# Kernel optimization log

Hardware: AMD Instinct MI355X
Metric: run time of the kernel (lower is better)

Reference implementation:

```python
import jax, jax.numpy as jnp
import numpy as np
from jax import lax

B, L, R = 128, 256, 36
D_TXT, D_IMG, D_SOC = 768, 2048, 10
EPS = 0.05 ** 2        # geomloss blur=0.05, p=2 -> epsilon = blur^p
N_ITERS = 20           # fixed log-domain Sinkhorn iterations
GAMMA = 0.01


def _pcost(x, y):
    # x: [B,n,d], y: [B,m,d] -> C_ij = ||x_i - y_j||^2 / 2 (geomloss p=2 cost)
    xx = jnp.sum(x * x, -1)[:, :, None]
    yy = jnp.sum(y * y, -1)[:, None, :]
    xy = jnp.einsum('bnd,bmd->bnm', x, y)
    return 0.5 * (xx + yy - 2.0 * xy)


def _sinkhorn_cost(C, loga, logb, eps, n_iters):
    # Log-domain Sinkhorn; masked points carry loga/logb = -inf (zero weight).
    f = jnp.zeros(loga.shape, C.dtype)
    g = jnp.zeros(logb.shape, C.dtype)

    def body(fg, _):
        f, g = fg
        g = -eps * jax.nn.logsumexp(loga[:, :, None] + (f[:, :, None] - C) / eps, axis=1)
        f = -eps * jax.nn.logsumexp(logb[:, None, :] + (g[:, None, :] - C) / eps, axis=2)
        return (f, g), None

    (f, g), _ = lax.scan(body, (f, g), None, length=n_iters)
    a = jnp.exp(loga)  # exp(-inf) = 0 for masked entries
    b = jnp.exp(logb)
    return jnp.sum(a * f, -1) + jnp.sum(b * g, -1)  # <a,f> + <b,g>


def _forward(txt_global, txt_region, img_global, img_region, social, attn_mask,
             W_stat, b_stat, W_gt, b_gt, W_gi, b_gi, W_rt, b_rt, W_ri, b_ri,
             W_m1, b_m1, W_m2, b_m2):
    relu = jax.nn.relu
    soc = relu(social @ W_stat + b_stat)                            # [B,100]
    tg = relu(jnp.concatenate([txt_global, soc], axis=1) @ W_gt + b_gt)  # [B,200]
    ig = relu(img_global @ W_gi + b_gi)                              # [B,200]
    h = relu((tg + ig) @ W_m1 + b_m1)
    mix_pred = h @ W_m2 + b_m2                                       # [B,2]

    tr = relu(txt_region @ W_rt + b_rt)                              # [B,L,50]
    ir = relu(img_region @ W_ri + b_ri)                              # [B,R,50]

    Bn, _, _ = tr.shape
    Rn = ir.shape[1]
    mask = attn_mask > 0
    n_words = jnp.sum(attn_mask, axis=-1).astype(tr.dtype)          # [B]
    loga = jnp.where(mask, -jnp.log(n_words)[:, None], -jnp.inf)    # uniform over valid tokens
    logb = jnp.full((Bn, Rn), -jnp.log(float(Rn)), tr.dtype)        # uniform over regions

    # Debiased Sinkhorn divergence (geomloss SamplesLoss default debias=True):
    Sxy = _sinkhorn_cost(_pcost(tr, ir), loga, logb, EPS, N_ITERS)
    Sxx = _sinkhorn_cost(_pcost(tr, tr), loga, loga, EPS, N_ITERS)
    Syy = _sinkhorn_cost(_pcost(ir, ir), logb, logb, EPS, N_ITERS)
    w_dis = Sxy - 0.5 * (Sxx + Syy)                                  # [B]

    w_pred = jnp.stack([1.0 - GAMMA * w_dis, GAMMA * w_dis], axis=1)  # [B,2]
    logit = jax.nn.softmax(jnp.maximum(mix_pred, w_pred), axis=1)
    return logit


def setup_inputs() -> dict:
    key = jax.random.key(0)
    ks = jax.random.split(key, 24)
    init = lambda k, s: (jax.random.normal(k, s) * 0.02).astype(jnp.float32)
    lengths = jax.random.randint(ks[0], (B,), 16, L + 1)             # ragged lengths
    attn_mask = (jnp.arange(L)[None, :] < lengths[:, None]).astype(jnp.int32)
    return {
        'txt_global': jax.random.normal(ks[1], (B, D_TXT), jnp.float32),
        'txt_region': jax.random.normal(ks[2], (B, L, D_TXT), jnp.float32),
        'img_global': jax.random.normal(ks[3], (B, D_IMG), jnp.float32),
        'img_region': jax.random.normal(ks[4], (B, R, D_IMG), jnp.float32),
        'social': jax.random.normal(ks[5], (B, D_SOC), jnp.float32),
        'attn_mask': attn_mask,
        'W_stat': init(ks[6], (D_SOC, 100)), 'b_stat': jnp.zeros((100,), jnp.float32),
        'W_gt': init(ks[7], (868, 200)), 'b_gt': jnp.zeros((200,), jnp.float32),
        'W_gi': init(ks[8], (D_IMG, 200)), 'b_gi': jnp.zeros((200,), jnp.float32),
        'W_rt': init(ks[9], (D_TXT, 50)), 'b_rt': jnp.zeros((50,), jnp.float32),
        'W_ri': init(ks[10], (D_IMG, 50)), 'b_ri': jnp.zeros((50,), jnp.float32),
        'W_m1': init(ks[11], (200, 100)), 'b_m1': jnp.zeros((100,), jnp.float32),
        'W_m2': init(ks[12], (100, 2)), 'b_m2': jnp.zeros((2,), jnp.float32),
    }


def reference(txt_global, txt_region, img_global, img_region, social, attn_mask,
              W_stat, b_stat, W_gt, b_gt, W_gi, b_gi, W_rt, b_rt, W_ri, b_ri,
              W_m1, b_m1, W_m2, b_m2):
    return _forward(txt_global, txt_region, img_global, img_region, social, attn_mask,
                    W_stat, b_stat, W_gt, b_gt, W_gi, b_gi, W_rt, b_rt, W_ri, b_ri,
                    W_m1, b_m1, W_m2, b_m2)
```

## Files before the change

### kernel.cpp

```cpp
#include <hip/hip_runtime.h>

typedef float  f32x4 __attribute__((ext_vector_type(4)));
typedef short  s16x8 __attribute__((ext_vector_type(8)));

#define EPS_LN2      0.0017328679513998632f
#define INV_EPS_LN2  577.0780163555852f
#define LOG2_36      5.169925001442312f

__device__ __forceinline__ short f2bf(float x) {
  unsigned int u; __builtin_memcpy(&u, &x, 4);
  u = (u + 0x7FFFu + ((u >> 16) & 1u)) >> 16;
  return (short)u;
}

#define GLOAD16(g, l) __builtin_amdgcn_global_load_lds( \
    (const __attribute__((address_space(1))) void*)(g), \
    (__attribute__((address_space(3))) void*)(l), 16, 0, 0)

__global__ __launch_bounds__(256) void k_prep(
    const float* __restrict__ W_rt, const float* __restrict__ W_ri,
    short* __restrict__ frt, short* __restrict__ fri,
    const float* __restrict__ txt, const float* __restrict__ img,
    const float* __restrict__ social,
    const float* __restrict__ W_stat, const float* __restrict__ b_stat,
    const float* __restrict__ W_gt, const float* __restrict__ W_gi,
    float* __restrict__ pre) {
  __shared__ float sA[32][128];
  int bid = blockIdx.x;
  if (bid < 88) {
    int slot = bid * 256 + threadIdx.x;
    const float* W; short* dst; int f;
    if (slot < 6144) { W = W_rt; dst = frt; f = slot; }
    else             { W = W_ri; dst = fri; f = slot - 6144; }
    int k32 = f >> 8, rem = f & 255, ct = rem >> 6, l = rem & 63;
    int col = ct * 16 + (l & 15);
    int k0  = k32 * 32 + (l >> 4) * 8;
    s16x8 p;
#pragma unroll
    for (int c = 0; c < 8; ++c) {
      float v = (col < 50) ? W[(k0 + c) * 50 + col] : 0.f;
      p[c] = f2bf(v);
    }
    *(s16x8*)(dst + (long)f * 8) = p;
    return;
  }
  int gb = bid - 88;
  int job = gb >> 4, rb = (gb >> 2) & 3, cb = gb & 3;
  int t = threadIdx.x, r0 = rb * 32;
  const float* W; int k0, klen;
  if (job < 6)       { k0 = job * 128;       klen = 128; W = W_gt; }
  else if (job == 6) { k0 = 0;               klen = 100; W = W_gt + 768 * 200; }
  else               { k0 = (job - 7) * 128; klen = 128; W = W_gi; }
  if (job == 6) {
    for (int idx = t; idx < 4096; idx += 256) {
      int r = idx >> 7, k = idx & 127;
      float v = 0.f;
      if (k < 100) {
        v = b_stat[k];
#pragma unroll
        for (int u = 0; u < 10; ++u) v += social[(r0 + r) * 10 + u] * W_stat[u * 100 + k];
        v = fmaxf(v, 0.f);
      }
      sA[r][k] = v;
    }
  } else {
    const float* A = (job < 6) ? txt : img;
    int K_A = (job < 6) ? 768 : 2048;
    for (int idx = t; idx < 4096; idx += 256) {
      int r = idx >> 7, k = idx & 127;
      sA[r][k] = A[(r0 + r) * K_A + k0 + k];
    }
  }
  __syncthreads();
  int c = cb * 64 + (t & 63), rg = t >> 6;
  if (c < 200) {
    float acc[8];
#pragma unroll
    for (int i = 0; i < 8; ++i) acc[i] = 0.f;
    for (int k4 = 0; k4 < klen; k4 += 4) {
      float w0 = W[(k0 + k4    ) * 200 + c];
      float w1 = W[(k0 + k4 + 1) * 200 + c];
      float w2 = W[(k0 + k4 + 2) * 200 + c];
      float w3 = W[(k0 + k4 + 3) * 200 + c];
#pragma unroll
      for (int i = 0; i < 8; ++i) {
        f32x4 a = *(const f32x4*)&sA[rg * 8 + i][k4];
        acc[i] += a[0]*w0 + a[1]*w1 + a[2]*w2 + a[3]*w3;
      }
    }
    float* dst = pre + (long)job * 25600;
#pragma unroll
    for (int i = 0; i < 8; ++i)
      dst[(r0 + rg * 8 + i) * 200 + c] = acc[i];
  }
}

template<int K32>
__device__ __forceinline__ void proj_body(const float* __restrict__ A,
                                          const short* __restrict__ Bf,
                                          const float* __restrict__ bias,
                                          float* __restrict__ out, int bid,
                                          char* smem) {
  char* abuf = smem;
  char* bbuf = smem + 16384;
  int wave = threadIdx.x >> 6, lane = threadIdx.x & 63;
  int rl = lane & 15, q = lane >> 4;
  int row0 = bid * 64;
  const int K = K32 * 32;
  const float* arow = A + (long)(row0 + wave * 16 + rl) * K + q * 8;
  const short* brow = Bf + wave * 512 + lane * 8;

#define PROJ_STAGE(KK, PH) { \
    const float* asrc = arow + (KK) * 32; \
    char* ad = abuf + (PH) * 8192 + wave * 2048; \
    GLOAD16(asrc,     ad); \
    GLOAD16(asrc + 4, ad + 1024); \
    GLOAD16(brow + (long)(KK) * 2048, bbuf + (PH) * 4096 + wave * 1024); \
  }

  f32x4 acc[4];
#pragma unroll
  for (int ct = 0; ct < 4; ++ct) acc[ct] = (f32x4){0.f, 0.f, 0.f, 0.f};

  PROJ_STAGE(0, 0);
  __syncthreads();

  for (int k = 0; k < K32; ++k) {
    if (k + 1 < K32) PROJ_STAGE(k + 1, (k + 1) & 1);
    const char* ab = abuf + (k & 1) * 8192 + wave * 2048 + lane * 16;
    const char* bb = bbuf + (k & 1) * 4096 + lane * 16;
    f32x4 a0 = *(const f32x4*)(ab);
    f32x4 a1 = *(const f32x4*)(ab + 1024);
    s16x8 af;
    af[0]=f2bf(a0[0]); af[1]=f2bf(a0[1]); af[2]=f2bf(a0[2]); af[3]=f2bf(a0[3]);
    af[4]=f2bf(a1[0]); af[5]=f2bf(a1[1]); af[6]=f2bf(a1[2]); af[7]=f2bf(a1[3]);
#pragma unroll
    for (int ct = 0; ct < 4; ++ct) {
      s16x8 bfr = *(const s16x8*)(bb + ct * 1024);
      acc[ct] = __builtin_amdgcn_mfma_f32_16x16x32_bf16(af, bfr, acc[ct], 0, 0, 0);
    }
    __syncthreads();
  }
#undef PROJ_STAGE

#pragma unroll
  for (int ct = 0; ct < 4; ++ct) {
    int col = ct * 16 + rl;
    float bv = (col < 50) ? bias[col] : 0.f;
#pragma unroll
    for (int r = 0; r < 4; ++r) {
      int grow = row0 + wave * 16 + q * 4 + r;
      float v = fmaxf(acc[ct][r] + bv, 0.f);
      out[(long)grow * 64 + col] = (col < 50) ? v : 0.f;
    }
  }
}

__device__ __forceinline__ void mix_body(
    int r, const float* __restrict__ pre,
    const float* __restrict__ b_gt, const float* __restrict__ b_gi,
    const float* __restrict__ W_m1, const float* __restrict__ b_m1,
    const float* __restrict__ W_m2, const float* __restrict__ b_m2,
    float* __restrict__ mix, float* smem) {
  float* sm = smem;
  float* sh = smem + 200;
  int t = threadIdx.x;
  if (t < 200) {
    float s1 = b_gt[t], s2 = b_gi[t];
#pragma unroll
    for (int j = 0; j < 7; ++j)  s1 += pre[(long)j * 25600 + r * 200 + t];
#pragma unroll
    for (int j = 7; j < 23; ++j) s2 += pre[(long)j * 25600 + r * 200 + t];
    sm[t] = fmaxf(s1, 0.f) + fmaxf(s2, 0.f);
  }
  __syncthreads();
  if (t < 100) {
    float a = b_m1[t];
#pragma unroll 4
    for (int k = 0; k < 200; ++k) a += sm[k] * W_m1[k * 100 + t];
    sh[t] = fmaxf(a, 0.f);
  }
  __syncthreads();
  if (t < 2) {
    float a = b_m2[t];
    for (int k = 0; k < 100; ++k) a += sh[k] * W_m2[k * 2 + t];
    mix[r * 2 + t] = a;
  }
}

__global__ __launch_bounds__(256)
void k_pm(
    const float* __restrict__ txt_region, const short* __restrict__ frt,
    const float* __restrict__ b_rt, float* __restrict__ tr,
    const float* __restrict__ img_region, const short* __restrict__ fri,
    const float* __restrict__ b_ri, float* __restrict__ ir,
    const float* __restrict__ pre,
    const float* __restrict__ b_gt, const float* __restrict__ b_gi,
    const float* __restrict__ W_m1, const float* __restrict__ b_m1,
    const float* __restrict__ W_m2, const float* __restrict__ b_m2,
    float* __restrict__ mix) {
  __shared__ __align__(16) char smem[24576];
  int bid = blockIdx.x;
  if (bid < 72)       proj_body<64>(img_region, fri, b_ri, ir, bid, smem);
  else if (bid < 584) proj_body<24>(txt_region, frt, b_rt, tr, bid - 72, smem);
  else                mix_body(bid - 584, pre, b_gt, b_gi, W_m1, b_m1, W_m2, b_m2, mix, (float*)smem);
}

#define SK_SMEM 50736

__global__ __launch_bounds__(1024)
__attribute__((amdgpu_waves_per_eu(4, 4)))
void k_sink(
    const float* __restrict__ tr, const float* __restrict__ ir,
    const int* __restrict__ amask, float* __restrict__ Cxx,
    float* __restrict__ Sxy, float* __restrict__ Sxx, float* __restrict__ Syy) {
  __shared__ __align__(16) char smem[SK_SMEM];
  int role = blockIdx.x >> 7;
  int b    = blockIdx.x & 127;
  int tid  = threadIdx.x;

  if (role == 0) {
    short* Xf    = (short*)smem;
    float* norms = (float*)(smem + 32768);
    float* sA    = (float*)(smem + 33792);
    float* sF    = (float*)(smem + 34816);
    float* sG    = (float*)(smem + 35840);
    float* sPm   = (float*)(smem + 36864);
    int*   nsh   = (int*)  (smem + 40960);
    if (tid < 64) {
      int c = 0;
      for (int i = tid; i < 256; i += 64) c += amask[b * 256 + i];
#pragma unroll
      for (int o = 1; o < 64; o <<= 1) c += __shfl_xor(c, o);
      if (tid == 0) *nsh = c;
    }
    const float* Xg = tr + (long)b * 256 * 64;
    for (int slot = tid; slot < 2048; slot += 1024) {
      int t = slot >> 7, k32 = (slot >> 6) & 1, l = slot & 63;
      int row = t * 16 + (l & 15), k0 = k32 * 32 + (l >> 4) * 8;
      const float* src = Xg + row * 64 + k0;
      f32x4 a0 = *(const f32x4*)src, a1 = *(const f32x4*)(src + 4);
      s16x8 p;
      p[0]=f2bf(a0[0]); p[1]=f2bf(a0[1]); p[2]=f2bf(a0[2]); p[3]=f2bf(a0[3]);
      p[4]=f2bf(a1[0]); p[5]=f2bf(a1[1]); p[6]=f2bf(a1[2]); p[7]=f2bf(a1[3]);
      *(s16x8*)(Xf + slot * 8) = p;
    }
    __syncthreads();
    int n = *nsh;
    int wv = tid >> 6, lane = tid & 63, q = lane >> 4;
    f32x4 acc[16];
#pragma unroll
    for (int ct = 0; ct < 16; ++ct) acc[ct] = (f32x4){0.f, 0.f, 0.f, 0.f};
    s16x8 afr0 = *(const s16x8*)(Xf + ((wv * 2 + 0) * 64 + lane) * 8);
    s16x8 afr1 = *(const s16x8*)(Xf + ((wv * 2 + 1) * 64 + lane) * 8);
#pragma unroll
    for (int ct = 0; ct < 16; ++ct) {
      s16x8 b0 = *(const s16x8*)(Xf + ((ct * 2 + 0) * 64 + lane) * 8);
      s16x8 b1 = *(const s16x8*)(Xf + ((ct * 2 + 1) * 64 + lane) * 8);
      acc[ct] = __builtin_amdgcn_mfma_f32_16x16x32_bf16(afr0, b0, acc[ct], 0, 0, 0);
      acc[ct] = __builtin_amdgcn_mfma_f32_16x16x32_bf16(afr1, b1, acc[ct], 0, 0, 0);
    }
#pragma unroll
    for (int r = 0; r < 4; ++r) {
      int m_ = q * 4 + r;
      if ((lane & 15) == m_) norms[wv * 16 + m_] = acc[wv][r];
    }
    __syncthreads();
    float* Cwb = Cxx + (long)b * 65536;
    if (wv * 16 < n) {
#pragma unroll
      for (int ct = 0; ct < 16; ++ct) {
        int gj = ct * 16 + (lane & 15);
        float nj = norms[gj];
#pragma unroll
        for (int r = 0; r < 4; ++r) {
          int gi = wv * 16 + q * 4 + r;
          Cwb[gi * 256 + gj] = (acc[ct][r] - 0.5f * (norms[gi] + nj)) * INV_EPS_LN2;
        }
      }
    }
    __syncthreads();
    int kk = tid >> 8, j = tid & 255, i0 = kk * 64;
    int iend = n - i0; if (iend > 64) iend = 64;
    f32x4 c0, c1, c2, c3, c4, c5, c6, c7, c8, c9, ca, cb, cc, cd, ce, cf;
    if (i0 < n) {
      const float* cp = Cwb + (long)i0 * 256 + j;
#define XXLD(CV, T0) \
      CV[0] = cp[(T0+0)*256]; CV[1] = cp[(T0+1)*256]; \
      CV[2] = cp[(T0+2)*256]; CV[3] = cp[(T0+3)*256];
      XXLD(c0, 0)  XXLD(c1, 4)  XXLD(c2, 8)  XXLD(c3, 12)
      XXLD(c4, 16) XXLD(c5, 20) XXLD(c6, 24) XXLD(c7, 28)
      XXLD(c8, 32) XXLD(c9, 36) XXLD(ca, 40) XXLD(cb, 44)
      XXLD(cc, 48) XXLD(cd, 52) XXLD(ce, 56) XXLD(cf, 60)
#undef XXLD
      asm volatile("" : "+v"(c0), "+v"(c1), "+v"(c2), "+v"(c3),
                        "+v"(c4), "+v"(c5), "+v"(c6), "+v"(c7),
                        "+v"(c8), "+v"(c9), "+v"(ca), "+v"(cb),
                        "+v"(cc), "+v"(cd), "+v"(ce), "+v"(cf));
    }
    float log2n = log2f((float)n);
    if (tid < 256) { sF[tid] = 0.f; sA[tid] = (tid < n) ? -log2n : -1e30f; }
    __syncthreads();
    const float* ap2 = sA + i0;
#define XXG(CA, CB, CC, CD, OFF) { \
      f32x4 A0 = *(const f32x4*)(ap2 + OFF); \
      f32x4 A1 = *(const f32x4*)(ap2 + OFF + 4); \
      f32x4 A2 = *(const f32x4*)(ap2 + OFF + 8); \
      f32x4 A3 = *(const f32x4*)(ap2 + OFF + 12); \
      float x0 = A0[0]+CA[0], x1 = A0[1]+CA[1], x2 = A0[2]+CA[2], x3 = A0[3]+CA[3]; \
      float x4 = A1[0]+CB[0], x5 = A1[1]+CB[1], x6 = A1[2]+CB[2], x7 = A1[3]+CB[3]; \
      float x8 = A2[0]+CC[0], x9 = A2[1]+CC[1], xa = A2[2]+CC[2], xb = A2[3]+CC[3]; \
      float xc = A3[0]+CD[0], xd = A3[1]+CD[1], xe = A3[2]+CD[2], xf = A3[3]+CD[3]; \
      float y0 = fmaxf(fmaxf(x0, x1), x2); \
      float y1 = fmaxf(fmaxf(x3, x4), x5); \
      float y2 = fmaxf(fmaxf(x6, x7), x8); \
      float y3 = fmaxf(fmaxf(x9, xa), xb); \
      float y4 = fmaxf(fmaxf(xc, xd), xe); \
      m = fmaxf(m, fmaxf(fmaxf(fmaxf(y0, y1), fmaxf(y2, y3)), fmaxf(y4, xf))); }
    for (int h = 0; h < 40; ++h) {
      float m = -1e30f;
      if (i0 < n && j < n) {
        XXG(c0, c1, c2, c3, 0)
        if (iend > 16) { XXG(c4, c5, c6, c7, 16) }
        if (iend > 32) { XXG(c8, c9, ca, cb, 32) }
        if (iend > 48) { XXG(cc, cd, ce, cf, 48) }
      }
      sPm[kk * 256 + j] = m;
      __syncthreads();
      if (tid < 256) {
        float m4 = fmaxf(fmaxf(sPm[tid], sPm[256 + tid]),
                         fmaxf(sPm[512 + tid], sPm[768 + tid]));
        if (tid < n) {
          ((h & 1) ? sF : sG)[tid] = -EPS_LN2 * m4;
          sA[tid] = -log2n - m4;
        }
      }
      __syncthreads();
    }
#undef XXG
    if (tid < 64) {
      float a = 0.f;
      for (int i = tid; i < n; i += 64) a += sF[i] + sG[i];
#pragma unroll
      for (int o = 1; o < 64; o <<= 1) a += __shfl_xor(a, o);
      if (tid == 0) Sxx[b] = a / n;
    }
  } else if (role == 1) {
    float* Ys  = (float*)smem;
    float* Cs  = (float*)(smem + 9216);
    float* nx  = (float*)(smem + 47104);
    float* ny  = (float*)(smem + 48128);
    float* sA  = (float*)(smem + 48288);
    float* sB  = (float*)(smem + 49376);
    float* sF  = (float*)(smem + 49536);
    float* sG  = (float*)(smem + 50560);
    int*   nsh = (int*)  (smem + 50720);
    if (tid < 64) {
      int c = 0;
      for (int i = tid; i < 256; i += 64) c += amask[b * 256 + i];
#pragma unroll
      for (int o = 1; o < 64; o <<= 1) c += __shfl_xor(c, o);
      if (tid == 0) *nsh = c;
    }
    const float* Xg = tr + (long)b * 256 * 64;
    const float* Yg = ir + (long)b * 36 * 64;
    for (int idx = tid; idx < 576; idx += 1024) {
      int row = idx >> 4, q4 = idx & 15;
      *(f32x4*)(Ys + row * 64 + q4 * 4) = *(const f32x4*)(Yg + row * 64 + q4 * 4);
    }
    __syncthreads();
    int n = *nsh;
    if (tid < 256) {
      float a = 0.f;
#pragma unroll
      for (int q4 = 0; q4 < 13; ++q4) {
        f32x4 v = *(const f32x4*)(Xg + tid * 64 + q4 * 4);
        a += v[0]*v[0] + v[1]*v[1] + v[2]*v[2] + v[3]*v[3];
      }
      nx[tid] = a;
    } else if (tid < 292) {
      int jj = tid - 256; float a = 0.f;
#pragma unroll
      for (int q4 = 0; q4 < 13; ++q4) {
        f32x4 v = *(const f32x4*)(Ys + jj * 64 + q4 * 4);
        a += v[0]*v[0] + v[1]*v[1] + v[2]*v[2] + v[3]*v[3];
      }
      ny[jj] = a;
    }
    __syncthreads();
    if (tid < 1008) {
      int ii = tid / 36, jj = tid - ii * 36;
      f32x4 yr[13];
#pragma unroll
      for (int q4 = 0; q4 < 13; ++q4) yr[q4] = *(const f32x4*)(Ys + jj * 64 + q4 * 4);
      float nyj = ny[jj];
      for (int i = ii; i < 256; i += 28) {
        float d = 0.f;
#pragma unroll
        for (int q4 = 0; q4 < 13; ++q4) {
          f32x4 xv = *(const f32x4*)(Xg + i * 64 + q4 * 4);
          d += xv[0]*yr[q4][0] + xv[1]*yr[q4][1] + xv[2]*yr[q4][2] + xv[3]*yr[q4][3];
        }
        Cs[i * 37 + jj] = (d - 0.5f * (nx[i] + nyj)) * INV_EPS_LN2;
      }
    }
    __syncthreads();
    int jg = tid >> 4, kg = tid & 15;
    float Cg[16];
    if (jg < 36) {
#pragma unroll
      for (int t = 0; t < 16; ++t) Cg[t] = Cs[(kg * 16 + t) * 37 + jg];
    }
    int fi = tid >> 2, kf = tid & 3;
    float Cf[9];
#pragma unroll
    for (int t = 0; t < 9; ++t) {
      int jj2 = kf * 9 + t;
      Cf[t] = (jj2 < 36) ? Cs[fi * 37 + jj2] : 0.f;
    }
    float log2n = log2f((float)n);
    if (tid < 256) { sF[tid] = 0.f; sA[tid + (tid >> 4)] = -log2n; }
    __syncthreads();
    const float* agp = sA + kg * 17;
    int gend = n - kg * 16; if (gend > 16) gend = 16;
    for (int it = 0; it < 20; ++it) {
      float gm = -1e30f;
      if (jg < 36) {
#pragma unroll
        for (int t = 0; t < 16; ++t)
          if (t < gend) gm = fmaxf(gm, agp[t] + Cg[t]);
        gm = fmaxf(gm, __shfl_xor(gm, 1)); gm = fmaxf(gm, __shfl_xor(gm, 2));
        gm = fmaxf(gm, __shfl_xor(gm, 4)); gm = fmaxf(gm, __shfl_xor(gm, 8));
      }
      __syncthreads();
      if (jg < 36 && kg == 0) {
        sG[jg] = -EPS_LN2 * gm;
        sB[jg] = -LOG2_36 - gm;
      }
      __syncthreads();
      float fm = -1e30f;
#pragma unroll
      for (int t = 0; t < 9; ++t) {
        int jj2 = kf * 9 + t;
        if (jj2 < 36) fm = fmaxf(fm, sB[jj2] + Cf[t]);
      }
      fm = fmaxf(fm, __shfl_xor(fm, 1)); fm = fmaxf(fm, __shfl_xor(fm, 2));
      __syncthreads();
      if (kf == 0 && fi < n) {
        sF[fi] = -EPS_LN2 * fm;
        sA[fi + (fi >> 4)] = -log2n - fm;
      }
      __syncthreads();
    }
    if (tid < 64) {
      float a = 0.f;
      for (int i = tid; i < n; i += 64) a += sF[i];
      float g = (tid < 36) ? sG[tid] : 0.f;
#pragma unroll
      for (int o = 1; o < 64; o <<= 1) { a += __shfl_xor(a, o); g += __shfl_xor(g, o); }
      if (tid == 0) Sxy[b] = a / n + g / 36.f;
    }
  } else {
    float* Ys = (float*)smem;
    float* Cs = (float*)(smem + 9216);
    float* ny = (float*)(smem + 48128);
    float* sA = (float*)(smem + 48288);
    float* sF = (float*)(smem + 49536);
    float* sG = (float*)(smem + 50560);
    const float* Yg = ir + (long)b * 36 * 64;
    for (int idx = tid; idx < 576; idx += 1024) {
      int row = idx >> 4, q4 = idx & 15;
      *(f32x4*)(Ys + row * 64 + q4 * 4) = *(const f32x4*)(Yg + row * 64 + q4 * 4);
    }
    __syncthreads();
    if (tid < 36) {
      float a = 0.f;
#pragma unroll
      for (int q4 = 0; q4 < 13; ++q4) {
        f32x4 v = *(const f32x4*)(Ys + tid * 64 + q4 * 4);
        a += v[0]*v[0] + v[1]*v[1] + v[2]*v[2] + v[3]*v[3];
      }
      ny[tid] = a;
    }
    __syncthreads();
    if (tid < 1008) {
      int ii = tid / 36, jj = tid - ii * 36;
      f32x4 yr[13];
#pragma unroll
      for (int q4 = 0; q4 < 13; ++q4) yr[q4] = *(const f32x4*)(Ys + jj * 64 + q4 * 4);
      float nyj = ny[jj];
      for (int i = ii; i < 36; i += 28) {
        float d = 0.f;
#pragma unroll
        for (int q4 = 0; q4 < 13; ++q4) {
          f32x4 xv = *(const f32x4*)(Ys + i * 64 + q4 * 4);
          d += xv[0]*yr[q4][0] + xv[1]*yr[q4][1] + xv[2]*yr[q4][2] + xv[3]*yr[q4][3];
        }
        Cs[i * 37 + jj] = (d - 0.5f * (ny[i] + nyj)) * INV_EPS_LN2;
      }
    }
    __syncthreads();
    int j = tid >> 2, kk = tid & 3;
    float Creg[9];
    if (j < 36) {
#pragma unroll
      for (int t = 0; t < 9; ++t) {
        int i2 = kk * 9 + t;
        Creg[t] = (i2 < 36) ? Cs[i2 * 37 + j] : 0.f;
      }
    }
    if (tid < 36) { sF[tid] = 0.f; sA[tid] = -LOG2_36; }
    __syncthreads();
    for (int h = 0; h < 40; ++h) {
      float m = -1e30f;
      if (j < 36) {
#pragma unroll
        for (int t = 0; t < 9; ++t) {
          int i2 = kk * 9 + t;
          if (i2 < 36) m = fmaxf(m, sA[i2] + Creg[t]);
        }
        m = fmaxf(m, __shfl_xor(m, 1)); m = fmaxf(m, __shfl_xor(m, 2));
      }
      __syncthreads();
      if (j < 36 && kk == 0) {
        ((h & 1) ? sF : sG)[j] = -EPS_LN2 * m;
        sA[j] = -LOG2_36 - m;
      }
      __syncthreads();
    }
    if (tid < 64) {
      float a = (tid < 36) ? sF[tid] + sG[tid] : 0.f;
#pragma unroll
      for (int o = 1; o < 64; o <<= 1) a += __shfl_xor(a, o);
      if (tid == 0) Syy[b] = a / 36.f;
    }
  }
}

__global__ void k_final(const float* __restrict__ mix, const float* __restrict__ sxy,
                        const float* __restrict__ sxx, const float* __restrict__ syy,
                        float* __restrict__ out) {
  int b = blockIdx.x * 64 + threadIdx.x;
  if (b < 128) {
    float w  = sxy[b] - 0.5f * (sxx[b] + syy[b]);
    float x0 = fmaxf(mix[b * 2 + 0], 1.0f - 0.01f * w);
    float x1 = fmaxf(mix[b * 2 + 1], 0.01f * w);
    float mx = fmaxf(x0, x1);
    float e0 = expf(x0 - mx), e1 = expf(x1 - mx);
    float inv = 1.f / (e0 + e1);
    out[b * 2 + 0] = e0 * inv;
    out[b * 2 + 1] = e1 * inv;
  }
}

extern "C" void kernel_launch(void* const* d_in, const int* in_sizes, int n_in,
                              void* d_out, int out_size, void* d_ws, size_t ws_size,
                              hipStream_t stream) {
  const float* txt_global = (const float*)d_in[0];
  const float* txt_region = (const float*)d_in[1];
  const float* img_global = (const float*)d_in[2];
  const float* img_region = (const float*)d_in[3];
  const float* social     = (const float*)d_in[4];
  const int*   attn_mask  = (const int*)  d_in[5];
  const float* W_stat = (const float*)d_in[6];  const float* b_stat = (const float*)d_in[7];
  const float* W_gt   = (const float*)d_in[8];  const float* b_gt   = (const float*)d_in[9];
  const float* W_gi   = (const float*)d_in[10]; const float* b_gi   = (const float*)d_in[11];
  const float* W_rt   = (const float*)d_in[12]; const float* b_rt   = (const float*)d_in[13];
  const float* W_ri   = (const float*)d_in[14]; const float* b_ri   = (const float*)d_in[15];
  const float* W_m1   = (const float*)d_in[16]; const float* b_m1   = (const float*)d_in[17];
  const float* W_m2   = (const float*)d_in[18]; const float* b_m2   = (const float*)d_in[19];

  float* ws = (float*)d_ws;
  float* ws_mix = ws;
  float* ws_sxy = ws + 256;
  float* ws_sxx = ws + 384;
  float* ws_syy = ws + 512;
  short* ws_frt = (short*)(ws + 1024);
  short* ws_fri = (short*)(ws + 25600);
  float* ws_tr  = ws + 131072;
  float* ws_ir  = ws + 2228224;
  float* ws_cxx = ws + 2523136;
  float* ws_pre = ws_cxx;

  k_prep<<<456, 256, 0, stream>>>(W_rt, W_ri, ws_frt, ws_fri,
                                  txt_global, img_global, social,
                                  W_stat, b_stat, W_gt, W_gi, ws_pre);
  k_pm<<<712, 256, 0, stream>>>(txt_region, ws_frt, b_rt, ws_tr,
                                img_region, ws_fri, b_ri, ws_ir,
                                ws_pre, b_gt, b_gi,
                                W_m1, b_m1, W_m2, b_m2, ws_mix);
  k_sink<<<384, 1024, 0, stream>>>(ws_tr, ws_ir, attn_mask, ws_cxx,
                                   ws_sxy, ws_sxx, ws_syy);
  k_final<<<2, 64, 0, stream>>>(ws_mix, ws_sxy, ws_sxx, ws_syy, (float*)d_out);
}
```

Baseline: 336.0 us.

## Split projection GEMM K across waves with direct global loads and LDS reduction

The region-projection kernel now gives each 256-thread block 16 rows instead of 64, and splits the K dimension across its four waves. Each wave loads A and B fragments straight from global memory instead of staging them in LDS, and the partial sums are combined through a small LDS reduction at the end. This quadruples the grid to expose more parallelism and removes the per-k-step block barriers. The cost is that B fragment reads are no longer shared across waves and the global-to-LDS async prefetch is gone. Occupancy hints also change: launch_bounds(256,8) on k_pm and a looser waves_per_eu range on the Sinkhorn kernel.

```diff
diff --git a/kernel.cpp b/kernel.cpp
--- a/kernel.cpp
+++ b/kernel.cpp
@@ -12,10 +12,6 @@
   u = (u + 0x7FFFu + ((u >> 16) & 1u)) >> 16;
   return (short)u;
 }
-
-#define GLOAD16(g, l) __builtin_amdgcn_global_load_lds( \
-    (const __attribute__((address_space(1))) void*)(g), \
-    (__attribute__((address_space(3))) void*)(l), 16, 0, 0)
 
 __global__ __launch_bounds__(256) void k_prep(
     const float* __restrict__ W_rt, const float* __restrict__ W_ri,
@@ -100,58 +96,54 @@
                                           const short* __restrict__ Bf,
                                           const float* __restrict__ bias,
                                           float* __restrict__ out, int bid,
-                                          char* smem) {
-  char* abuf = smem;
-  char* bbuf = smem + 16384;
+                                          f32x4* __restrict__ red) {
+  constexpr int KQ = K32 / 4;
   int wave = threadIdx.x >> 6, lane = threadIdx.x & 63;
   int rl = lane & 15, q = lane >> 4;
-  int row0 = bid * 64;
+  int row0 = bid * 16;
   const int K = K32 * 32;
-  const float* arow = A + (long)(row0 + wave * 16 + rl) * K + q * 8;
-  const short* brow = Bf + wave * 512 + lane * 8;
-
-#define PROJ_STAGE(KK, PH) { \
-    const float* asrc = arow + (KK) * 32; \
-    char* ad = abuf + (PH) * 8192 + wave * 2048; \
-    GLOAD16(asrc,     ad); \
-    GLOAD16(asrc + 4, ad + 1024); \
-    GLOAD16(brow + (long)(KK) * 2048, bbuf + (PH) * 4096 + wave * 1024); \
-  }
+  const float* ar = A + (long)(row0 + rl) * K + wave * (KQ * 32) + q * 8;
+  const s16x8* bp = (const s16x8*)Bf + wave * (KQ * 256) + lane;
 
   f32x4 acc[4];
 #pragma unroll
   for (int ct = 0; ct < 4; ++ct) acc[ct] = (f32x4){0.f, 0.f, 0.f, 0.f};
 
-  PROJ_STAGE(0, 0);
-  __syncthreads();
-
-  for (int k = 0; k < K32; ++k) {
-    if (k + 1 < K32) PROJ_STAGE(k + 1, (k + 1) & 1);
-    const char* ab = abuf + (k & 1) * 8192 + wave * 2048 + lane * 16;
-    const char* bb = bbuf + (k & 1) * 4096 + lane * 16;
-    f32x4 a0 = *(const f32x4*)(ab);
-    f32x4 a1 = *(const f32x4*)(ab + 1024);
+#pragma unroll 2
+  for (int k = 0; k < KQ; ++k) {
+    f32x4 a0 = *(const f32x4*)(ar + k * 32);
+    f32x4 a1 = *(const f32x4*)(ar + k * 32 + 4);
+    const s16x8* p = bp + k * 256;
+    s16x8 b0 = p[0], b1 = p[64], b2 = p[128], b3 = p[192];
     s16x8 af;
     af[0]=f2bf(a0[0]); af[1]=f2bf(a0[1]); af[2]=f2bf(a0[2]); af[3]=f2bf(a0[3]);
     af[4]=f2bf(a1[0]); af[5]=f2bf(a1[1]); af[6]=f2bf(a1[2]); af[7]=f2bf(a1[3]);
+    acc[0] = __builtin_amdgcn_mfma_f32_16x16x32_bf16(af, b0, acc[0], 0, 0, 0);
+    acc[1] = __builtin_amdgcn_mfma_f32_16x16x32_bf16(af, b1, acc[1], 0, 0, 0);
+    acc[2] = __builtin_amdgcn_mfma_f32_16x16x32_bf16(af, b2, acc[2], 0, 0, 0);
+    acc[3] = __builtin_amdgcn_mfma_f32_16x16x32_bf16(af, b3, acc[3], 0, 0, 0);
+  }
+
+  if (wave) {
+#pragma unroll
+    for (int ct = 0; ct < 4; ++ct)
+      red[((wave - 1) * 4 + ct) * 64 + lane] = acc[ct];
+  }
+  __syncthreads();
+  if (wave == 0) {
 #pragma unroll
     for (int ct = 0; ct < 4; ++ct) {
-      s16x8 bfr = *(const s16x8*)(bb + ct * 1024);
-      acc[ct] = __builtin_amdgcn_mfma_f32_16x16x32_bf16(af, bfr, acc[ct], 0, 0, 0);
-    }
-    __syncthreads();
-  }
-#undef PROJ_STAGE
-
-#pragma unroll
-  for (int ct = 0; ct < 4; ++ct) {
-    int col = ct * 16 + rl;
-    float bv = (col < 50) ? bias[col] : 0.f;
-#pragma unroll
-    for (int r = 0; r < 4; ++r) {
-      int grow = row0 + wave * 16 + q * 4 + r;
-      float v = fmaxf(acc[ct][r] + bv, 0.f);
-      out[(long)grow * 64 + col] = (col < 50) ? v : 0.f;
+      f32x4 s = acc[ct];
+#pragma unroll
+      for (int w = 0; w < 3; ++w) s = s + red[(w * 4 + ct) * 64 + lane];
+      int col = ct * 16 + rl;
+      float bv = (col < 50) ? bias[col] : 0.f;
+#pragma unroll
+      for (int r = 0; r < 4; ++r) {
+        int grow = row0 + q * 4 + r;
+        float v = fmaxf(s[r] + bv, 0.f);
+        out[(long)grow * 64 + col] = (col < 50) ? v : 0.f;
+      }
     }
   }
 }
@@ -188,7 +180,7 @@
   }
 }
 
-__global__ __launch_bounds__(256)
+__global__ __launch_bounds__(256, 8)
 void k_pm(
     const float* __restrict__ txt_region, const short* __restrict__ frt,
     const float* __restrict__ b_rt, float* __restrict__ tr,
@@ -199,17 +191,17 @@
     const float* __restrict__ W_m1, const float* __restrict__ b_m1,
     const float* __restrict__ W_m2, const float* __restrict__ b_m2,
     float* __restrict__ mix) {
-  __shared__ __align__(16) char smem[24576];
+  __shared__ __align__(16) f32x4 red[768];
   int bid = blockIdx.x;
-  if (bid < 72)       proj_body<64>(img_region, fri, b_ri, ir, bid, smem);
-  else if (bid < 584) proj_body<24>(txt_region, frt, b_rt, tr, bid - 72, smem);
-  else                mix_body(bid - 584, pre, b_gt, b_gi, W_m1, b_m1, W_m2, b_m2, mix, (float*)smem);
+  if (bid < 288)       proj_body<64>(img_region, fri, b_ri, ir, bid, red);
+  else if (bid < 2336) proj_body<24>(txt_region, frt, b_rt, tr, bid - 288, red);
+  else                 mix_body(bid - 2336, pre, b_gt, b_gi, W_m1, b_m1, W_m2, b_m2, mix, (float*)red);
 }
 
 #define SK_SMEM 50736
 
 __global__ __launch_bounds__(1024)
-__attribute__((amdgpu_waves_per_eu(4, 4)))
+__attribute__((amdgpu_waves_per_eu(4, 12)))
 void k_sink(
     const float* __restrict__ tr, const float* __restrict__ ir,
     const int* __restrict__ amask, float* __restrict__ Cxx,
@@ -585,10 +577,10 @@
   k_prep<<<456, 256, 0, stream>>>(W_rt, W_ri, ws_frt, ws_fri,
                                   txt_global, img_global, social,
                                   W_stat, b_stat, W_gt, W_gi, ws_pre);
-  k_pm<<<712, 256, 0, stream>>>(txt_region, ws_frt, b_rt, ws_tr,
-                                img_region, ws_fri, b_ri, ws_ir,
-                                ws_pre, b_gt, b_gi,
-                                W_m1, b_m1, W_m2, b_m2, ws_mix);
+  k_pm<<<2464, 256, 0, stream>>>(txt_region, ws_frt, b_rt, ws_tr,
+                                 img_region, ws_fri, b_ri, ws_ir,
+                                 ws_pre, b_gt, b_gi,
+                                 W_m1, b_m1, W_m2, b_m2, ws_mix);
   k_sink<<<384, 1024, 0, stream>>>(ws_tr, ws_ir, attn_mask, ws_cxx,
                                    ws_sxy, ws_sxx, ws_syy);
   k_final<<<2, 64, 0, stream>>>(ws_mix, ws_sxy, ws_sxx, ws_syy, (float*)d_out);
```

New measurement: 327.3 us. -2.6%, faster.
